# Performance work log

Measured on AMD Instinct MI355X. Metric: run time of the kernel, lower is better.

## Reference

```python
import jax, jax.numpy as jnp
import numpy as np

E = 8   # num routed experts
K = 1   # top-k per token
D = 512   # embed_dim
I = 2048  # moe_inter_dim (= 4*D)
B, T = 2, 2048


def setup_inputs() -> dict:
    key = jax.random.key(0)
    ks = jax.random.split(key, 7)
    s = 0.02
    x = jax.random.normal(ks[0], (B, T, D), jnp.float32)
    gate_w = jax.random.normal(ks[1], (E, D), jnp.float32) * s      # TopKGate.proj.weight
    w1 = jax.random.normal(ks[2], (E, I, D), jnp.float32) * s       # Expert.w1.weight per expert
    w2 = jax.random.normal(ks[3], (E, D, I), jnp.float32) * s       # Expert.w2.weight
    w3 = jax.random.normal(ks[4], (E, I, D), jnp.float32) * s       # Expert.w3.weight
    sw1 = jax.random.normal(ks[5], (I, D), jnp.float32) * s         # shared Linear(dim -> 1*inter)
    sw2 = jax.random.normal(ks[6], (D, I), jnp.float32) * s         # shared Linear(inter -> dim)
    return {"x": x, "gate_w": gate_w, "w1": w1, "w2": w2, "w3": w3, "sw1": sw1, "sw2": sw2}


def reference(x, gate_w, w1, w2, w3, sw1, sw2):
    xf = x.reshape(-1, D)                                  # [N, D]
    # gate: logits -> topk -> softmax over selected logits
    logits = xf @ gate_w.T                                 # [N, E]
    wts, idx = jax.lax.top_k(logits, K)                    # [N, K]
    wts = jax.nn.softmax(wts, axis=-1)
    # per-token combine weight for each expert (0 if not routed) -- identical
    # math to the torch gather/scatter loop, fully vectorized over experts.
    comb = jnp.einsum('nke,nk->ne', jax.nn.one_hot(idx, E, dtype=xf.dtype), wts)  # [N, E]
    # SwiGLU experts, batched over the expert axis
    h = jax.nn.silu(jnp.einsum('nd,eid->nei', xf, w1)) * jnp.einsum('nd,eid->nei', xf, w3)  # [N, E, I]
    y = jnp.einsum('nei,edi->nd', h * comb[:, :, None], w2)  # weighted combine
    # shared expert: Linear -> GELU(exact) -> Linear
    y = y + jax.nn.gelu(xf @ sw1.T, approximate=False) @ sw2.T
    return y.reshape(x.shape)
```

## Files before the change

### kernel.cpp

```cpp
#include <hip/hip_runtime.h>
#include <hip/hip_bf16.h>
#include <math.h>

#define N_TOK 4096
#define DIM 512
#define IDIM 2048
#define NEXP 8

#define W1_ELS 8388608
#define W3_ELS 8388608
#define W2_ELS 8388608
#define SW1_ELS 1048576
#define SW2_ELS 1048576
#define CONV_ELS 27262976
#define CONV_CHUNKS 3407872
#define GATE_BLOCKS 256
#define CONV_BLOCKS 2048
#define CONV_THREADS (CONV_BLOCKS * 256)

typedef __attribute__((ext_vector_type(8))) short bf16x8;
typedef __attribute__((ext_vector_type(4))) float floatx4;

__device__ __forceinline__ short f2bf(float f) {
  unsigned int u;
  __builtin_memcpy(&u, &f, 4);
  u += 0x7fff + ((u >> 16) & 1);
  return (short)(u >> 16);
}

__device__ __forceinline__ bf16x8 ld8f(const float* __restrict__ p) {
  float4 a = *(const float4*)p;
  float4 b = *(const float4*)(p + 4);
  bf16x8 v;
  v[0] = f2bf(a.x); v[1] = f2bf(a.y); v[2] = f2bf(a.z); v[3] = f2bf(a.w);
  v[4] = f2bf(b.x); v[5] = f2bf(b.y); v[6] = f2bf(b.z); v[7] = f2bf(b.w);
  return v;
}

__device__ __forceinline__ float gelu_exactish(float v) {
  float z = fabsf(v) * 0.70710678118f;
  float tt = 1.f / (1.f + 0.3275911f * z);
  float poly = tt * (0.254829592f + tt * (-0.284496736f + tt * (1.421413741f +
               tt * (-1.453152027f + tt * 1.061405429f))));
  float er = 1.f - poly * __expf(-z * z);
  er = (v < 0.f) ? -er : er;
  return 0.5f * v * (1.f + er);
}

__device__ __forceinline__ void gll(const short* g, short* l) {
  __builtin_amdgcn_global_load_lds(
      (const __attribute__((address_space(1))) void*)g,
      (__attribute__((address_space(3))) void*)l, 16, 0, 0);
}

__global__ __launch_bounds__(256) void gate_conv_kernel(
    const float* __restrict__ x, const float* __restrict__ gw,
    short* __restrict__ xb, int* __restrict__ expert_id,
    const float* __restrict__ w1, const float* __restrict__ w3,
    const float* __restrict__ w2, const float* __restrict__ sw1,
    const float* __restrict__ sw2,
    short* __restrict__ w1b, short* __restrict__ w3b, short* __restrict__ w2b,
    short* __restrict__ sw1b, short* __restrict__ sw2b) {
  __shared__ float xs[16 * 516];
  __shared__ double ps[16][8][2];
  int t = threadIdx.x;

  if (blockIdx.x >= GATE_BLOCKS) {
    long tidg = (long)(blockIdx.x - GATE_BLOCKS) * 256 + t;
    for (long c = tidg; c < CONV_CHUNKS; c += CONV_THREADS) {
      long i = c * 8;
      const float* src;
      short* dst;
      long off;
      if (i < W1_ELS)                          { src = w1;  dst = w1b;  off = i; }
      else if (i < 2L * W1_ELS)                { src = w3;  dst = w3b;  off = i - W1_ELS; }
      else if (i < 3L * W1_ELS)                { src = w2;  dst = w2b;  off = i - 2L * W1_ELS; }
      else if (i < 3L * W1_ELS + SW1_ELS)      { src = sw1; dst = sw1b; off = i - 3L * W1_ELS; }
      else                                     { src = sw2; dst = sw2b; off = i - 3L * W1_ELS - SW1_ELS; }
      *(bf16x8*)(dst + off) = ld8f(src + off);
    }
    return;
  }

  int tok0 = blockIdx.x * 16;
  const float* xrow = x + (long)tok0 * DIM;
  for (int i = t; i < 2048; i += 256) {
    float4 v = ((const float4*)xrow)[i];
    int row = i >> 7, c4 = i & 127;
    *(float4*)&xs[row * 516 + c4 * 4] = v;
    short4 b;
    b.x = f2bf(v.x); b.y = f2bf(v.y); b.z = f2bf(v.z); b.w = f2bf(v.w);
    *(short4*)(xb + (long)tok0 * DIM + i * 4) = b;
  }
  __syncthreads();
  int tok = t & 15, e = (t >> 4) & 7, hf = t >> 7;
  const float* xr = &xs[tok * 516 + hf * 256];
  const float* wr = gw + e * DIM + hf * 256;
  double s = 0.0;
  for (int k = 0; k < 256; k += 4) {
    float4 xv = *(const float4*)(xr + k);
    float4 wv = *(const float4*)(wr + k);
    s += (double)xv.x * wv.x + (double)xv.y * wv.y +
         (double)xv.z * wv.z + (double)xv.w * wv.w;
  }
  ps[tok][e][hf] = s;
  __syncthreads();
  if (t < 16) {
    double best = ps[t][0][0] + ps[t][0][1];
    int bi = 0;
#pragma unroll
    for (int j = 1; j < 8; j++) {
      double v = ps[t][j][0] + ps[t][j][1];
      if (v > best) { best = v; bi = j; }
    }
    expert_id[tok0 + t] = bi;
  }
}

__global__ __launch_bounds__(256) void scan_scatter(
    const int* __restrict__ expert_id, int* __restrict__ counts,
    int* __restrict__ offsets, int* __restrict__ cursors, int* __restrict__ nmeta,
    int* __restrict__ te1, int* __restrict__ tr1,
    int* __restrict__ te2, int* __restrict__ tr2, int* __restrict__ perm) {
  __shared__ int cnt[8];
  __shared__ int scur[8];
  int tid = threadIdx.x;
  if (tid < 8) cnt[tid] = 0;
  __syncthreads();
  int eid[16];
#pragma unroll
  for (int j = 0; j < 16; j++) {
    eid[j] = expert_id[tid + j * 256];
    atomicAdd(&cnt[eid[j]], 1);
  }
  __syncthreads();
  if (tid == 0) {
    int acc = 0;
    for (int e = 0; e < NEXP; e++) {
      counts[e] = cnt[e];
      offsets[e] = acc;
      scur[e] = acc;
      acc += cnt[e];
    }
    int n1 = 0;
    for (int e = 0; e < NEXP; e++)
      for (int r = 0; r < cnt[e]; r += 64) { te1[n1] = e; tr1[n1] = r; n1++; }
    for (int r = 0; r < N_TOK; r += 64) { te1[n1] = 8; tr1[n1] = r; n1++; }
    int n2 = 0;
    for (int e = 0; e < NEXP; e++)
      for (int r = 0; r < cnt[e]; r += 64) { te2[n2] = e; tr2[n2] = r; n2++; }
    nmeta[0] = n1;
    nmeta[1] = n2;
  }
  __syncthreads();
#pragma unroll
  for (int j = 0; j < 16; j++) {
    int slot = atomicAdd(&scur[eid[j]], 1);
    perm[slot] = tid + j * 256;
  }
}

__global__ __launch_bounds__(256, 3) void stage1(
    const short* __restrict__ xb, const short* __restrict__ w1b,
    const short* __restrict__ w3b, const short* __restrict__ sw1b,
    short* __restrict__ h, short* __restrict__ g,
    const int* __restrict__ counts, const int* __restrict__ offsets,
    const int* __restrict__ nmeta, const int* __restrict__ te,
    const int* __restrict__ tr, const int* __restrict__ perm) {
  __shared__ short Al0[64 * 64];
  __shared__ short Al1[64 * 64];
  __shared__ short B1l0[64 * 64];
  __shared__ short B1l1[64 * 64];
  __shared__ short B2l0[64 * 64];
  __shared__ short B2l1[64 * 64];
  int t = blockIdx.y;
  if (t >= nmeta[0]) return;
  int e = te[t], row0 = tr[t];
  bool routed = (e < 8);
  int cnt = routed ? counts[e] : N_TOK;
  int base = routed ? offsets[e] : 0;
  int n0 = blockIdx.x * 64;
  int tid = threadIdx.x, lane = tid & 63, w = tid >> 6;
  int wm = w >> 1, wn = w & 1;
  const short* B1 = routed ? w1b + (long)e * IDIM * DIM : sw1b;
  const short* B2 = w3b + (long)e * IDIM * DIM;

  int aoff[2], bgoff[2], lb[2];
#pragma unroll
  for (int i = 0; i < 2; i++) {
    int c = i * 256 + tid;
    int row = c >> 3, klog = (c & 7) ^ (row & 7);
    int srow = row0 + row;
    int slot = base + ((srow < cnt) ? srow : (cnt - 1));
    aoff[i] = perm[slot] * DIM + klog * 8;
    bgoff[i] = (n0 + row) * DIM + klog * 8;
    lb[i] = (i * 256 + w * 64) * 8;
  }

  floatx4 acc[2][2][2];
#pragma unroll
  for (int m = 0; m < 2; m++)
#pragma unroll
    for (int i = 0; i < 2; i++)
#pragma unroll
      for (int j = 0; j < 2; j++) acc[m][i][j] = (floatx4)0.f;

#pragma unroll
  for (int i = 0; i < 2; i++) gll(xb + aoff[i], &Al0[lb[i]]);
#pragma unroll
  for (int i = 0; i < 2; i++) gll(B1 + bgoff[i], &B1l0[lb[i]]);
  if (routed) {
#pragma unroll
    for (int i = 0; i < 2; i++) gll(B2 + bgoff[i], &B2l0[lb[i]]);
  }
  __syncthreads();

#pragma unroll
  for (int ki = 0; ki < 8; ki++) {
    const int kc = ki * 64;
    short* An = (ki & 1) ? Al0 : Al1;
    short* B1n = (ki & 1) ? B1l0 : B1l1;
    short* B2n = (ki & 1) ? B2l0 : B2l1;
    const short* Ac = (ki & 1) ? Al1 : Al0;
    const short* B1c = (ki & 1) ? B1l1 : B1l0;
    const short* B2c = (ki & 1) ? B2l1 : B2l0;

    if (ki < 7) {
#pragma unroll
      for (int i = 0; i < 2; i++) gll(xb + aoff[i] + kc + 64, &An[lb[i]]);
#pragma unroll
      for (int i = 0; i < 2; i++) gll(B1 + bgoff[i] + kc + 64, &B1n[lb[i]]);
      if (routed) {
#pragma unroll
        for (int i = 0; i < 2; i++) gll(B2 + bgoff[i] + kc + 64, &B2n[lb[i]]);
      }
    }

#pragma unroll
    for (int kf = 0; kf < 2; kf++) {
      int kp = (kf * 4 + (lane >> 4)) ^ (lane & 7);
      bf16x8 af[2];
#pragma unroll
      for (int mf = 0; mf < 2; mf++) {
        int row = wm * 32 + mf * 16 + (lane & 15);
        af[mf] = *(const bf16x8*)&Ac[row * 64 + kp * 8];
      }
#pragma unroll
      for (int nf = 0; nf < 2; nf++) {
        int col = wn * 32 + nf * 16 + (lane & 15);
        bf16x8 b1 = *(const bf16x8*)&B1c[col * 64 + kp * 8];
#pragma unroll
        for (int mf = 0; mf < 2; mf++)
          acc[0][mf][nf] = __builtin_amdgcn_mfma_f32_16x16x32_bf16(
              af[mf], b1, acc[0][mf][nf], 0, 0, 0);
        if (routed) {
          bf16x8 b2 = *(const bf16x8*)&B2c[col * 64 + kp * 8];
#pragma unroll
          for (int mf = 0; mf < 2; mf++)
            acc[1][mf][nf] = __builtin_amdgcn_mfma_f32_16x16x32_bf16(
                af[mf], b2, acc[1][mf][nf], 0, 0, 0);
        }
      }
    }
    __syncthreads();
  }

  short* S = Al0;
  int quad = lane >> 4;
  short* dst = routed ? h : g;
#pragma unroll
  for (int mf = 0; mf < 2; mf++)
#pragma unroll
    for (int r = 0; r < 4; r++) {
      int lr = wm * 32 + mf * 16 + quad * 4 + r;
      int sw = ((lr >> 2) & 3) << 4;
#pragma unroll
      for (int nf = 0; nf < 2; nf++) {
        int lc = wn * 32 + nf * 16 + (lane & 15);
        float a1 = acc[0][mf][nf][r];
        short v;
        if (routed) {
          float a3 = acc[1][mf][nf][r];
          v = f2bf((a1 / (1.f + __expf(-a1))) * a3);
        } else {
          v = f2bf(gelu_exactish(a1));
        }
        S[lr * 64 + ((lc & 48) ^ sw) + (lc & 15)] = v;
      }
    }
  __syncthreads();
  {
    int lr = tid >> 2;
    int srow = row0 + lr;
    if (srow < cnt) {
      int p = (tid & 3) * 16;
      int lcs = p ^ (((lr >> 2) & 3) << 4);
      bf16x8 v0 = *(const bf16x8*)&S[lr * 64 + lcs];
      bf16x8 v1 = *(const bf16x8*)&S[lr * 64 + lcs + 8];
      long ro = (long)(base + srow) * IDIM + n0 + p;
      *(bf16x8*)&dst[ro] = v0;
      *(bf16x8*)&dst[ro + 8] = v1;
    }
  }
}

__global__ __launch_bounds__(256, 8) void stage2(
    const short* __restrict__ h, const short* __restrict__ g,
    const short* __restrict__ w2b, const short* __restrict__ sw2b,
    float* __restrict__ out, const int* __restrict__ counts,
    const int* __restrict__ offsets, const int* __restrict__ nmeta,
    const int* __restrict__ te, const int* __restrict__ tr,
    const int* __restrict__ perm) {
  __shared__ short Al[64 * 64];
  __shared__ short Bl[32 * 64];
  int lid = blockIdx.x + 16 * blockIdx.y;
  int logical = (lid & 7) * 144 + (lid >> 3);
  int t = logical >> 4;
  int n0 = (logical & 15) * 32;
  if (t >= nmeta[1]) return;
  int e = te[t], row0 = tr[t];
  int cnt = counts[e], base = offsets[e];
  const short* w2e = w2b + (long)e * DIM * IDIM;
  int tid = threadIdx.x, lane = tid & 63, w = tid >> 6;
  int wm = w >> 1, wn = w & 1;

  int aoff[2], lbA[2];
#pragma unroll
  for (int i = 0; i < 2; i++) {
    int c = i * 256 + tid;
    int row = c >> 3, klog = (c & 7) ^ (row & 7);
    int srow = row0 + row;
    int arow = base + ((srow < cnt) ? srow : (cnt - 1));
    aoff[i] = arow * IDIM + klog * 8;
    lbA[i] = (i * 256 + w * 64) * 8;
  }
  int brow = tid >> 3, bklog = (tid & 7) ^ (brow & 7);
  int bgoff = (n0 + brow) * IDIM + bklog * 8;
  int lbB = (w * 64) * 8;

  floatx4 acc[2];
  acc[0] = (floatx4)0.f;
  acc[1] = (floatx4)0.f;

#pragma unroll
  for (int ph = 0; ph < 2; ph++) {
    const short* As = ph ? g : h;
    const short* Bs = ph ? sw2b : w2e;
    for (int kc = 0; kc < IDIM; kc += 64) {
#pragma unroll
      for (int i = 0; i < 2; i++) gll(As + aoff[i] + kc, &Al[lbA[i]]);
      gll(Bs + bgoff + kc, &Bl[lbB]);
      __syncthreads();

#pragma unroll
      for (int kf = 0; kf < 2; kf++) {
        int kp = (kf * 4 + (lane >> 4)) ^ (lane & 7);
        int col = wn * 16 + (lane & 15);
        bf16x8 bv = *(const bf16x8*)&Bl[col * 64 + kp * 8];
#pragma unroll
        for (int mf = 0; mf < 2; mf++) {
          int row = wm * 32 + mf * 16 + (lane & 15);
          bf16x8 af = *(const bf16x8*)&Al[row * 64 + kp * 8];
          acc[mf] = __builtin_amdgcn_mfma_f32_16x16x32_bf16(
              af, bv, acc[mf], 0, 0, 0);
        }
      }
      __syncthreads();
    }
  }

  int quad = lane >> 4;
  int colb = n0 + wn * 16 + (lane & 15);
#pragma unroll
  for (int mf = 0; mf < 2; mf++)
#pragma unroll
    for (int r = 0; r < 4; r++) {
      int srow = row0 + wm * 32 + mf * 16 + quad * 4 + r;
      if (srow >= cnt) continue;
      long ro = (long)perm[base + srow] * DIM + colb;
      out[ro] = acc[mf][r];
    }
}

extern "C" void kernel_launch(void* const* d_in, const int* in_sizes, int n_in,
                              void* d_out, int out_size, void* d_ws, size_t ws_size,
                              hipStream_t stream) {
  const float* x = (const float*)d_in[0];
  const float* gate_w = (const float*)d_in[1];
  const float* w1 = (const float*)d_in[2];
  const float* w2 = (const float*)d_in[3];
  const float* w3 = (const float*)d_in[4];
  const float* sw1 = (const float*)d_in[5];
  const float* sw2 = (const float*)d_in[6];
  float* out = (float*)d_out;

  char* ws = (char*)d_ws;
  int* counts = (int*)ws;
  int* offsets = counts + 8;
  int* cursors = offsets + 8;
  int* nmeta = cursors + 8;
  int* te1 = nmeta + 8;
  int* tr1 = te1 + 256;
  int* te2 = tr1 + 256;
  int* tr2 = te2 + 256;
  int* expert_id = tr2 + 256;
  int* perm = expert_id + N_TOK;
  short* xb = (short*)(ws + 65536);
  short* h = xb + (size_t)N_TOK * DIM;
  short* g = h + (size_t)N_TOK * IDIM;
  short* w1b = g + (size_t)N_TOK * IDIM;
  short* w3b = w1b + (size_t)W1_ELS;
  short* w2b = w3b + (size_t)W3_ELS;
  short* sw1b = w2b + (size_t)W2_ELS;
  short* sw2b = sw1b + (size_t)SW1_ELS;

  gate_conv_kernel<<<GATE_BLOCKS + CONV_BLOCKS, 256, 0, stream>>>(
      x, gate_w, xb, expert_id, w1, w3, w2, sw1, sw2,
      w1b, w3b, w2b, sw1b, sw2b);
  scan_scatter<<<1, 256, 0, stream>>>(expert_id, counts, offsets, cursors, nmeta,
                                      te1, tr1, te2, tr2, perm);
  stage1<<<dim3(IDIM / 64, 136), 256, 0, stream>>>(
      xb, w1b, w3b, sw1b, h, g, counts, offsets, nmeta, te1, tr1, perm);
  stage2<<<dim3(16, 72), 256, 0, stream>>>(
      h, g, w2b, sw2b, out, counts, offsets, nmeta, te2, tr2, perm);
}
```

Before: 242.4 us.

## Double-buffer LDS tiles in stage2 to overlap global loads with MFMA

Stage2's K-loop now uses two LDS buffers per operand. The next tile is prefetched with global-to-LDS loads while MFMAs run on the current one, and the two phases (routed expert and shared expert) are fused into one 64-step loop. This hides global load latency and drops one barrier per step. In exchange LDS use doubles and the occupancy hint falls from 8 to 4 blocks per CU.

New measurement: 251.9 us. 3.9% more time.

```diff
diff --git a/kernel.cpp b/kernel.cpp
--- a/kernel.cpp
+++ b/kernel.cpp
@@ -304,15 +304,17 @@
   }
 }
 
-__global__ __launch_bounds__(256, 8) void stage2(
+__global__ __launch_bounds__(256, 4) void stage2(
     const short* __restrict__ h, const short* __restrict__ g,
     const short* __restrict__ w2b, const short* __restrict__ sw2b,
     float* __restrict__ out, const int* __restrict__ counts,
     const int* __restrict__ offsets, const int* __restrict__ nmeta,
     const int* __restrict__ te, const int* __restrict__ tr,
     const int* __restrict__ perm) {
-  __shared__ short Al[64 * 64];
-  __shared__ short Bl[32 * 64];
+  __shared__ short Al0[64 * 64];
+  __shared__ short Al1[64 * 64];
+  __shared__ short Bl0[32 * 64];
+  __shared__ short Bl1[32 * 64];
   int lid = blockIdx.x + 16 * blockIdx.y;
   int logical = (lid & 7) * 144 + (lid >> 3);
   int t = logical >> 4;
@@ -342,32 +344,42 @@
   acc[0] = (floatx4)0.f;
   acc[1] = (floatx4)0.f;
 
-#pragma unroll
-  for (int ph = 0; ph < 2; ph++) {
-    const short* As = ph ? g : h;
-    const short* Bs = ph ? sw2b : w2e;
-    for (int kc = 0; kc < IDIM; kc += 64) {
-#pragma unroll
-      for (int i = 0; i < 2; i++) gll(As + aoff[i] + kc, &Al[lbA[i]]);
-      gll(Bs + bgoff + kc, &Bl[lbB]);
-      __syncthreads();
-
-#pragma unroll
-      for (int kf = 0; kf < 2; kf++) {
-        int kp = (kf * 4 + (lane >> 4)) ^ (lane & 7);
-        int col = wn * 16 + (lane & 15);
-        bf16x8 bv = *(const bf16x8*)&Bl[col * 64 + kp * 8];
-#pragma unroll
-        for (int mf = 0; mf < 2; mf++) {
-          int row = wm * 32 + mf * 16 + (lane & 15);
-          bf16x8 af = *(const bf16x8*)&Al[row * 64 + kp * 8];
-          acc[mf] = __builtin_amdgcn_mfma_f32_16x16x32_bf16(
-              af, bv, acc[mf], 0, 0, 0);
-        }
-      }
-      __syncthreads();
-    }
-  }
+#define S2_PF(s, An, Bn)                                                  \
+  if ((s) < 64) {                                                         \
+    const short* As_ = ((s) < 32) ? h : g;                                \
+    const short* Bs_ = ((s) < 32) ? w2e : sw2b;                           \
+    int kc_ = ((s) & 31) * 64;                                            \
+    _Pragma("unroll")                                                     \
+    for (int i = 0; i < 2; i++) gll(As_ + aoff[i] + kc_, &(An)[lbA[i]]);  \
+    gll(Bs_ + bgoff + kc_, &(Bn)[lbB]);                                   \
+  }
+#define S2_CP(Ac, Bc)                                                     \
+  _Pragma("unroll")                                                       \
+  for (int kf = 0; kf < 2; kf++) {                                        \
+    int kp = (kf * 4 + (lane >> 4)) ^ (lane & 7);                         \
+    int col = wn * 16 + (lane & 15);                                      \
+    bf16x8 bv = *(const bf16x8*)&(Bc)[col * 64 + kp * 8];                 \
+    _Pragma("unroll")                                                     \
+    for (int mf = 0; mf < 2; mf++) {                                      \
+      int row = wm * 32 + mf * 16 + (lane & 15);                          \
+      bf16x8 af = *(const bf16x8*)&(Ac)[row * 64 + kp * 8];               \
+      acc[mf] = __builtin_amdgcn_mfma_f32_16x16x32_bf16(                  \
+          af, bv, acc[mf], 0, 0, 0);                                      \
+    }                                                                     \
+  }
+
+  S2_PF(0, Al0, Bl0);
+  __syncthreads();
+  for (int s = 0; s < 64; s += 2) {
+    S2_PF(s + 1, Al1, Bl1);
+    S2_CP(Al0, Bl0);
+    __syncthreads();
+    S2_PF(s + 2, Al0, Bl0);
+    S2_CP(Al1, Bl1);
+    __syncthreads();
+  }
+#undef S2_PF
+#undef S2_CP
 
   int quad = lane >> 4;
   int colb = n0 + wn * 16 + (lane & 15);
```
